# Kernel tuning notes

Measured on AMD Instinct MI355X. Metric: run time of the kernel, lower is better.

The kernel has to match this reference:

```python
import jax, jax.numpy as jnp
import numpy as np

MASK_VALUE = -1000000.0  # matches sequence_mask fill in the torch source


def setup_inputs() -> dict:
    key = jax.random.key(0)
    k1, k2, k3, k4 = jax.random.split(key, 4)
    B, Lq, Lk, D = 64, 1024, 1024, 64
    return {
        "queries": jax.random.normal(k1, (B, Lq, D), dtype=jnp.float32),
        "keys": jax.random.normal(k2, (B, Lk, D), dtype=jnp.float32),
        "values": jax.random.normal(k3, (B, Lk, D), dtype=jnp.float32),
        "valid_lens": jax.random.randint(k4, (B,), 1, Lk + 1, dtype=jnp.int64),
    }


def reference(queries, keys, values, valid_lens):
    # queries: [B, Lq, D], keys/values: [B, Lk, D], valid_lens: [B]
    d = queries.shape[-1]
    qk = jnp.einsum("bqd,bkd->bqk", queries, keys) / jnp.sqrt(jnp.asarray(d, queries.dtype))
    # sequence_mask: positions >= valid_len are set to -1e6 before softmax.
    # valid_lens is per-batch-row, broadcast over queries (repeat_interleave in torch).
    kpos = jnp.arange(keys.shape[1])  # [Lk]
    mask = kpos[None, None, :] < valid_lens[:, None, None]  # [B, 1, Lk] -> broadcast over q
    qk = jnp.where(mask, qk, jnp.asarray(MASK_VALUE, qk.dtype))
    attn = jax.nn.softmax(qk, axis=-1)
    return jnp.einsum("bqk,bkd->bqd", attn, values)
```

## Files before the change

### kernel.cpp

```cpp
#include <hip/hip_runtime.h>
#include <hip/hip_bf16.h>


#define NB    64
#define LQ    1024
#define LK    1024
#define DH    64
#define KVT   64
#define QT    128
#define NITEMS (NB * (LQ / QT))
#define NEGF  1.0e30f
#define SC2   0.18033688011112042f
#define THR   8.0f

typedef __attribute__((ext_vector_type(8))) short    bf8;
typedef __attribute__((ext_vector_type(8))) ushort   u16x8;
typedef __attribute__((ext_vector_type(4))) ushort   u16x4;
typedef __attribute__((ext_vector_type(4))) float    f4;

__device__ __forceinline__ ushort2 cvt2(float a, float b) {
    float2 f; f.x = a; f.y = b;
    __hip_bfloat162 h = __float22bfloat162_rn(f);
    union { __hip_bfloat162 h2; ushort2 u2; } u;
    u.h2 = h;
    return u.u2;
}
__device__ __forceinline__ int swz16(int row, int colbyte) {
    return row * 128 + ((((colbyte >> 4) ^ (row & 7)) << 4) | (colbyte & 15));
}
__device__ __forceinline__ int swz8(int row, int colbyte) {
    return row * 128 + ((((colbyte >> 3) ^ (row & 15)) << 3) | (colbyte & 7));
}

__global__ __launch_bounds__(512, 4)
void attn_v16(const float* __restrict__ Q, const float* __restrict__ K,
              const float* __restrict__ V, const int* __restrict__ VL,
              float* __restrict__ O) {
    __shared__ ushort KsB[2][KVT * DH];
    __shared__ ushort VtB[2][DH * KVT];
    __shared__ ushort sched[NB];

    const int tid = threadIdx.x;
    const int wid = tid >> 6, l = tid & 63, g = l >> 4, a = l & 15;

    if (tid < NB) {
        const int ntb = (VL[tid] + KVT - 1) >> 6;
        int r = 0;
        for (int j = 0; j < NB; ++j) {
            const int ntj = (VL[j] + KVT - 1) >> 6;
            r += (int)((ntj > ntb) | ((ntj == ntb) & (j < tid)));
        }
        sched[r] = (ushort)tid;
    }
    __syncthreads();
    const int xcd   = blockIdx.x & 7;
    const int slot  = blockIdx.x >> 3;
    const int qtile = slot & 7;
    const int st    = slot >> 3;
    const int rank  = xcd + ((st < 4) ? st : (11 - st)) * 8;
    const int b     = sched[rank];
    const int qbase = qtile * QT;
    const int valid = VL[b];
    const int nt = (valid + KVT - 1) >> 6;

    const float* Qr = Q + ((size_t)b * LQ + qbase + wid * 16 + a) * DH;
    bf8 qa[2];
    #pragma unroll
    for (int kblk = 0; kblk < 2; ++kblk) {
        f4 x = *(const f4*)(Qr + kblk * 32 + g * 8);
        f4 y = *(const f4*)(Qr + kblk * 32 + g * 8 + 4);
        ushort2 c0 = cvt2(x[0] * SC2, x[1] * SC2), c1 = cvt2(x[2] * SC2, x[3] * SC2);
        ushort2 c2 = cvt2(y[0] * SC2, y[1] * SC2), c3 = cvt2(y[2] * SC2, y[3] * SC2);
        qa[kblk][0] = (short)c0.x; qa[kblk][1] = (short)c0.y;
        qa[kblk][2] = (short)c1.x; qa[kblk][3] = (short)c1.y;
        qa[kblk][4] = (short)c2.x; qa[kblk][5] = (short)c2.y;
        qa[kblk][6] = (short)c3.x; qa[kblk][7] = (short)c3.y;
    }
    const bf8 ones = {0x3F80, 0x3F80, 0x3F80, 0x3F80,
                      0x3F80, 0x3F80, 0x3F80, 0x3F80};

    const int  rtid  = tid & 255;
    const bool vrole = (wid < 4);
    const int srow = rtid >> 3, sslot = rtid & 7;
    const int vkp  = rtid >> 4, vj = rtid & 15;
    const int prow = (srow & 3) | ((srow & 24) >> 1) | ((srow & 4) << 2);
    const f4* Kb4 = (const f4*)(K + (size_t)b * LK * DH);
    const f4* Vb4 = (const f4*)(V + (size_t)b * LK * DH);

    f4 r0, r1, r2, r3;
    auto load_kv = [&](int k0) {
        if (vrole) {
            r0 = Vb4[(k0 + 4 * vkp + 0) * 16 + vj];
            r1 = Vb4[(k0 + 4 * vkp + 1) * 16 + vj];
            r2 = Vb4[(k0 + 4 * vkp + 2) * 16 + vj];
            r3 = Vb4[(k0 + 4 * vkp + 3) * 16 + vj];
        } else {
            r0 = Kb4[(k0 + srow) * 16 + sslot * 2];
            r1 = Kb4[(k0 + srow) * 16 + sslot * 2 + 1];
            r2 = Kb4[(k0 + srow + 32) * 16 + sslot * 2];
            r3 = Kb4[(k0 + srow + 32) * 16 + sslot * 2 + 1];
        }
    };
    auto store_kv = [&](int bs) {
        if (vrole) {
            char* vd = (char*)&VtB[bs][0];
            #pragma unroll
            for (int c = 0; c < 4; ++c) {
                ushort2 a01 = cvt2(r0[c], r1[c]), a23 = cvt2(r2[c], r3[c]);
                u16x4 p = {a01.x, a01.y, a23.x, a23.y};
                *(u16x4*)(vd + swz8(4 * vj + c, vkp * 8)) = p;
            }
        } else {
            char* kd = (char*)&KsB[bs][0];
            {
                ushort2 c0 = cvt2(r0[0], r0[1]), c1 = cvt2(r0[2], r0[3]);
                ushort2 c2 = cvt2(r1[0], r1[1]), c3 = cvt2(r1[2], r1[3]);
                u16x8 w = {c0.x, c0.y, c1.x, c1.y, c2.x, c2.y, c3.x, c3.y};
                *(u16x8*)(kd + swz16(prow, sslot * 16)) = w;
            }
            {
                ushort2 c0 = cvt2(r2[0], r2[1]), c1 = cvt2(r2[2], r2[3]);
                ushort2 c2 = cvt2(r3[0], r3[1]), c3 = cvt2(r3[2], r3[3]);
                u16x8 w = {c0.x, c0.y, c1.x, c1.y, c2.x, c2.y, c3.x, c3.y};
                *(u16x8*)(kd + swz16(prow + 32, sslot * 16)) = w;
            }
        }
    };

    f4 oacc[4];
    #pragma unroll
    for (int n = 0; n < 4; ++n) oacc[n] = f4{0.f, 0.f, 0.f, 0.f};
    f4 lacc = f4{0.f, 0.f, 0.f, 0.f};
    float m_run = -NEGF;

    load_kv(0);
    store_kv(0);
    for (int t = 0; t < nt; ++t) {
        const int bs = t & 1;
        __syncthreads();
        if (t + 1 < nt) load_kv((t + 1) * KVT);
        __builtin_amdgcn_sched_barrier(0);

        const char* kd = (const char*)&KsB[bs][0];
        f4 sacc[4];
        #pragma unroll
        for (int n = 0; n < 4; ++n) sacc[n] = f4{0.f, 0.f, 0.f, 0.f};
        __builtin_amdgcn_s_setprio(1);
        #pragma unroll
        for (int n = 0; n < 4; ++n)
            #pragma unroll
            for (int kblk = 0; kblk < 2; ++kblk) {
                bf8 kb = *(const bf8*)(kd + swz16(n * 16 + a, kblk * 64 + g * 16));
                sacc[n] = __builtin_amdgcn_mfma_f32_16x16x32_bf16(
                    kb, qa[kblk], sacc[n], 0, 0, 0);
            }
        __builtin_amdgcn_s_setprio(0);

        float s[4][4];
        const int kmax = valid - t * KVT;
        #pragma unroll
        for (int n = 0; n < 4; ++n)
            #pragma unroll
            for (int r = 0; r < 4; ++r) s[n][r] = sacc[n][r];
        if (kmax < KVT) {
            #pragma unroll
            for (int n = 0; n < 4; ++n)
                #pragma unroll
                for (int r = 0; r < 4; ++r)
                    if (32 * (n >> 1) + 4 * (n & 1) + 8 * g + r >= kmax)
                        s[n][r] = -NEGF;
        }

        float tm = s[0][0];
        #pragma unroll
        for (int n = 0; n < 4; ++n)
            #pragma unroll
            for (int r = 0; r < 4; ++r) tm = fmaxf(tm, s[n][r]);
        tm = fmaxf(tm, __shfl_xor(tm, 16));
        tm = fmaxf(tm, __shfl_xor(tm, 32));

        float rs_ = 1.0f;
        const bool skip = __all(tm <= m_run + THR);
        if (!skip) {
            const float mnew = fmaxf(m_run, tm);
            rs_ = __builtin_exp2f(m_run - mnew);
            m_run = mnew;
        }

        float p[4][4];
        #pragma unroll
        for (int n = 0; n < 4; ++n)
            #pragma unroll
            for (int r = 0; r < 4; ++r)
                p[n][r] = __builtin_exp2f(s[n][r] - m_run);

        if (!skip) {
            float rr[4];
            #pragma unroll
            for (int r = 0; r < 4; ++r) rr[r] = __shfl(rs_, 4 * g + r);
            #pragma unroll
            for (int n = 0; n < 4; ++n)
                #pragma unroll
                for (int r = 0; r < 4; ++r) oacc[n][r] *= rr[r];
            #pragma unroll
            for (int r = 0; r < 4; ++r) lacc[r] *= rr[r];
        }

        const char* vd = (const char*)&VtB[bs][0];
        __builtin_amdgcn_s_setprio(1);
        #pragma unroll
        for (int kblk = 0; kblk < 2; ++kblk) {
            ushort2 w0 = cvt2(p[2 * kblk][0], p[2 * kblk][1]);
            ushort2 w1 = cvt2(p[2 * kblk][2], p[2 * kblk][3]);
            ushort2 w2 = cvt2(p[2 * kblk + 1][0], p[2 * kblk + 1][1]);
            ushort2 w3 = cvt2(p[2 * kblk + 1][2], p[2 * kblk + 1][3]);
            bf8 pa = {(short)w0.x, (short)w0.y, (short)w1.x, (short)w1.y,
                      (short)w2.x, (short)w2.y, (short)w3.x, (short)w3.y};
            const int cb = kblk * 64 + g * 16;
            #pragma unroll
            for (int n = 0; n < 4; ++n) {
                u16x4 lo = *(const u16x4*)(vd + swz8(n * 16 + a, cb));
                u16x4 hi = *(const u16x4*)(vd + swz8(n * 16 + a, cb + 8));
                bf8 vb_ = {(short)lo[0], (short)lo[1], (short)lo[2], (short)lo[3],
                           (short)hi[0], (short)hi[1], (short)hi[2], (short)hi[3]};
                oacc[n] = __builtin_amdgcn_mfma_f32_16x16x32_bf16(
                    pa, vb_, oacc[n], 0, 0, 0);
            }
            lacc = __builtin_amdgcn_mfma_f32_16x16x32_bf16(pa, ones, lacc, 0, 0, 0);
        }
        __builtin_amdgcn_s_setprio(0);

        if (t + 1 < nt) store_kv(bs ^ 1);
    }

    float iv[4];
    #pragma unroll
    for (int r = 0; r < 4; ++r) iv[r] = 1.0f / lacc[r];
    float* Ob = O + ((size_t)b * LQ + qbase + wid * 16) * DH;
    #pragma unroll
    for (int n = 0; n < 4; ++n)
        #pragma unroll
        for (int r = 0; r < 4; ++r)
            Ob[(size_t)(4 * g + r) * DH + 16 * n + a] = oacc[n][r] * iv[r];
}

extern "C" void kernel_launch(void* const* d_in, const int* in_sizes, int n_in,
                              void* d_out, int out_size, void* d_ws, size_t ws_size,
                              hipStream_t stream) {
    const float* Q  = (const float*)d_in[0];
    const float* K  = (const float*)d_in[1];
    const float* V  = (const float*)d_in[2];
    const int*   VL = (const int*)d_in[3];
    float* O = (float*)d_out;

    attn_v16<<<NITEMS, 512, 0, stream>>>(Q, K, V, VL, O);
}
```

Before: 33.59 us.

## Software-pipeline QK of next tile with PV of current tile

Restructures the main loop so the QK^T MFMA for tile t+1 runs right after tile t's softmax, interleaved with tile t's PV MFMA. The prologue computes the first QK, and KV loads are prefetched two tiles ahead. The aim is to let matrix work overlap the softmax exponent and reduction work. The cost is an extra barrier per iteration and more live registers. The row-max reduction is also rewritten as a balanced tree.

New measurement: 38.32 us. 1.14x slower.

```diff
diff --git a/kernel.cpp b/kernel.cpp
--- a/kernel.cpp
+++ b/kernel.cpp
@@ -33,7 +33,7 @@
 }
 
 __global__ __launch_bounds__(512, 4)
-void attn_v16(const float* __restrict__ Q, const float* __restrict__ K,
+void attn_v18(const float* __restrict__ Q, const float* __restrict__ K,
               const float* __restrict__ V, const int* __restrict__ VL,
               float* __restrict__ O) {
     __shared__ ushort KsB[2][KVT * DH];
@@ -127,25 +127,11 @@
         }
     };
 
-    f4 oacc[4];
-    #pragma unroll
-    for (int n = 0; n < 4; ++n) oacc[n] = f4{0.f, 0.f, 0.f, 0.f};
-    f4 lacc = f4{0.f, 0.f, 0.f, 0.f};
-    float m_run = -NEGF;
-
-    load_kv(0);
-    store_kv(0);
-    for (int t = 0; t < nt; ++t) {
-        const int bs = t & 1;
-        __syncthreads();
-        if (t + 1 < nt) load_kv((t + 1) * KVT);
-        __builtin_amdgcn_sched_barrier(0);
-
-        const char* kd = (const char*)&KsB[bs][0];
-        f4 sacc[4];
+    f4 sacc[4];
+    auto do_qk = [&](int bufK) {
+        const char* kd = (const char*)&KsB[bufK][0];
         #pragma unroll
         for (int n = 0; n < 4; ++n) sacc[n] = f4{0.f, 0.f, 0.f, 0.f};
-        __builtin_amdgcn_s_setprio(1);
         #pragma unroll
         for (int n = 0; n < 4; ++n)
             #pragma unroll
@@ -154,8 +140,24 @@
                 sacc[n] = __builtin_amdgcn_mfma_f32_16x16x32_bf16(
                     kb, qa[kblk], sacc[n], 0, 0, 0);
             }
-        __builtin_amdgcn_s_setprio(0);
-
+    };
+
+    f4 oacc[4];
+    #pragma unroll
+    for (int n = 0; n < 4; ++n) oacc[n] = f4{0.f, 0.f, 0.f, 0.f};
+    f4 lacc = f4{0.f, 0.f, 0.f, 0.f};
+    float m_run = -NEGF;
+
+    load_kv(0);
+    store_kv(0);
+    __syncthreads();
+    __builtin_amdgcn_s_setprio(1);
+    do_qk(0);
+    __builtin_amdgcn_s_setprio(0);
+    if (nt > 1) load_kv(KVT);
+
+    for (int t = 0; t < nt; ++t) {
+        const int bs = t & 1;
         float s[4][4];
         const int kmax = valid - t * KVT;
         #pragma unroll
@@ -171,11 +173,11 @@
                         s[n][r] = -NEGF;
         }
 
-        float tm = s[0][0];
-        #pragma unroll
-        for (int n = 0; n < 4; ++n)
-            #pragma unroll
-            for (int r = 0; r < 4; ++r) tm = fmaxf(tm, s[n][r]);
+        float m0 = fmaxf(fmaxf(s[0][0], s[0][1]), fmaxf(s[0][2], s[0][3]));
+        float m1 = fmaxf(fmaxf(s[1][0], s[1][1]), fmaxf(s[1][2], s[1][3]));
+        float m2 = fmaxf(fmaxf(s[2][0], s[2][1]), fmaxf(s[2][2], s[2][3]));
+        float m3 = fmaxf(fmaxf(s[3][0], s[3][1]), fmaxf(s[3][2], s[3][3]));
+        float tm = fmaxf(fmaxf(m0, m1), fmaxf(m2, m3));
         tm = fmaxf(tm, __shfl_xor(tm, 16));
         tm = fmaxf(tm, __shfl_xor(tm, 32));
 
@@ -206,16 +208,30 @@
             for (int r = 0; r < 4; ++r) lacc[r] *= rr[r];
         }
 
-        const char* vd = (const char*)&VtB[bs][0];
-        __builtin_amdgcn_s_setprio(1);
+        bf8 pa[2];
         #pragma unroll
         for (int kblk = 0; kblk < 2; ++kblk) {
             ushort2 w0 = cvt2(p[2 * kblk][0], p[2 * kblk][1]);
             ushort2 w1 = cvt2(p[2 * kblk][2], p[2 * kblk][3]);
             ushort2 w2 = cvt2(p[2 * kblk + 1][0], p[2 * kblk + 1][1]);
             ushort2 w3 = cvt2(p[2 * kblk + 1][2], p[2 * kblk + 1][3]);
-            bf8 pa = {(short)w0.x, (short)w0.y, (short)w1.x, (short)w1.y,
-                      (short)w2.x, (short)w2.y, (short)w3.x, (short)w3.y};
+            pa[kblk][0] = (short)w0.x; pa[kblk][1] = (short)w0.y;
+            pa[kblk][2] = (short)w1.x; pa[kblk][3] = (short)w1.y;
+            pa[kblk][4] = (short)w2.x; pa[kblk][5] = (short)w2.y;
+            pa[kblk][6] = (short)w3.x; pa[kblk][7] = (short)w3.y;
+        }
+
+        if (t + 1 < nt) store_kv(bs ^ 1);
+
+        __syncthreads();
+        if (t + 2 < nt) load_kv((t + 2) * KVT);
+        __builtin_amdgcn_sched_barrier(0);
+        __builtin_amdgcn_s_setprio(1);
+        if (t + 1 < nt) do_qk(bs ^ 1);
+
+        const char* vd = (const char*)&VtB[bs][0];
+        #pragma unroll
+        for (int kblk = 0; kblk < 2; ++kblk) {
             const int cb = kblk * 64 + g * 16;
             #pragma unroll
             for (int n = 0; n < 4; ++n) {
@@ -224,13 +240,12 @@
                 bf8 vb_ = {(short)lo[0], (short)lo[1], (short)lo[2], (short)lo[3],
                            (short)hi[0], (short)hi[1], (short)hi[2], (short)hi[3]};
                 oacc[n] = __builtin_amdgcn_mfma_f32_16x16x32_bf16(
-                    pa, vb_, oacc[n], 0, 0, 0);
-            }
-            lacc = __builtin_amdgcn_mfma_f32_16x16x32_bf16(pa, ones, lacc, 0, 0, 0);
+                    pa[kblk], vb_, oacc[n], 0, 0, 0);
+            }
+            lacc = __builtin_amdgcn_mfma_f32_16x16x32_bf16(pa[kblk], ones, lacc, 0, 0, 0);
         }
         __builtin_amdgcn_s_setprio(0);
-
-        if (t + 1 < nt) store_kv(bs ^ 1);
+        __syncthreads();
     }
 
     float iv[4];
@@ -253,5 +268,5 @@
     const int*   VL = (const int*)d_in[3];
     float* O = (float*)d_out;
 
-    attn_v16<<<NITEMS, 512, 0, stream>>>(Q, K, V, VL, O);
-}
+    attn_v18<<<NITEMS, 512, 0, stream>>>(Q, K, V, VL, O);
+}
```

## Process two 64-key KV tiles per loop iteration to halve barriers

Applied to the files above, without the earlier changes.

Each loop iteration now loads, converts and stores 128 keys/values (two 64-row halves) and computes scores and PV over both, so each barrier and online-softmax max/rescale step covers twice as much work. The exp computation is fused into the PV loop per k-block. This is meant to cut synchronisation and softmax overhead per key. In exchange it doubles LDS use (64KB per block) and register pressure, which may hurt occupancy under the 4-blocks launch bound. It also rounds the key count up to a multiple of 128, relying on masking for the extra 64-key half.

Result: slower. 38.17 us (+13.6%).

```diff
diff --git a/kernel.cpp b/kernel.cpp
--- a/kernel.cpp
+++ b/kernel.cpp
@@ -7,6 +7,7 @@
 #define LK    1024
 #define DH    64
 #define KVT   64
+#define KVP   128
 #define QT    128
 #define NITEMS (NB * (LQ / QT))
 #define NEGF  1.0e30f
@@ -33,11 +34,11 @@
 }
 
 __global__ __launch_bounds__(512, 4)
-void attn_v16(const float* __restrict__ Q, const float* __restrict__ K,
+void attn_v19(const float* __restrict__ Q, const float* __restrict__ K,
               const float* __restrict__ V, const int* __restrict__ VL,
               float* __restrict__ O) {
-    __shared__ ushort KsB[2][KVT * DH];
-    __shared__ ushort VtB[2][DH * KVT];
+    __shared__ ushort KsB[2][2][KVT * DH];
+    __shared__ ushort VtB[2][2][DH * KVT];
     __shared__ ushort sched[NB];
 
     const int tid = threadIdx.x;
@@ -62,19 +63,20 @@
     const int qbase = qtile * QT;
     const int valid = VL[b];
     const int nt = (valid + KVT - 1) >> 6;
+    const int nu = (nt + 1) >> 1;
 
     const float* Qr = Q + ((size_t)b * LQ + qbase + wid * 16 + a) * DH;
     bf8 qa[2];
     #pragma unroll
-    for (int kblk = 0; kblk < 2; ++kblk) {
-        f4 x = *(const f4*)(Qr + kblk * 32 + g * 8);
-        f4 y = *(const f4*)(Qr + kblk * 32 + g * 8 + 4);
+    for (int dk = 0; dk < 2; ++dk) {
+        f4 x = *(const f4*)(Qr + dk * 32 + g * 8);
+        f4 y = *(const f4*)(Qr + dk * 32 + g * 8 + 4);
         ushort2 c0 = cvt2(x[0] * SC2, x[1] * SC2), c1 = cvt2(x[2] * SC2, x[3] * SC2);
         ushort2 c2 = cvt2(y[0] * SC2, y[1] * SC2), c3 = cvt2(y[2] * SC2, y[3] * SC2);
-        qa[kblk][0] = (short)c0.x; qa[kblk][1] = (short)c0.y;
-        qa[kblk][2] = (short)c1.x; qa[kblk][3] = (short)c1.y;
-        qa[kblk][4] = (short)c2.x; qa[kblk][5] = (short)c2.y;
-        qa[kblk][6] = (short)c3.x; qa[kblk][7] = (short)c3.y;
+        qa[dk][0] = (short)c0.x; qa[dk][1] = (short)c0.y;
+        qa[dk][2] = (short)c1.x; qa[dk][3] = (short)c1.y;
+        qa[dk][4] = (short)c2.x; qa[dk][5] = (short)c2.y;
+        qa[dk][6] = (short)c3.x; qa[dk][7] = (short)c3.y;
     }
     const bf8 ones = {0x3F80, 0x3F80, 0x3F80, 0x3F80,
                       0x3F80, 0x3F80, 0x3F80, 0x3F80};
@@ -87,44 +89,56 @@
     const f4* Kb4 = (const f4*)(K + (size_t)b * LK * DH);
     const f4* Vb4 = (const f4*)(V + (size_t)b * LK * DH);
 
-    f4 r0, r1, r2, r3;
-    auto load_kv = [&](int k0) {
+    f4 r0, r1, r2, r3, r4, r5, r6, r7;
+    auto load_kv2 = [&](int k0) {
         if (vrole) {
             r0 = Vb4[(k0 + 4 * vkp + 0) * 16 + vj];
             r1 = Vb4[(k0 + 4 * vkp + 1) * 16 + vj];
             r2 = Vb4[(k0 + 4 * vkp + 2) * 16 + vj];
             r3 = Vb4[(k0 + 4 * vkp + 3) * 16 + vj];
+            r4 = Vb4[(k0 + 64 + 4 * vkp + 0) * 16 + vj];
+            r5 = Vb4[(k0 + 64 + 4 * vkp + 1) * 16 + vj];
+            r6 = Vb4[(k0 + 64 + 4 * vkp + 2) * 16 + vj];
+            r7 = Vb4[(k0 + 64 + 4 * vkp + 3) * 16 + vj];
         } else {
             r0 = Kb4[(k0 + srow) * 16 + sslot * 2];
             r1 = Kb4[(k0 + srow) * 16 + sslot * 2 + 1];
             r2 = Kb4[(k0 + srow + 32) * 16 + sslot * 2];
             r3 = Kb4[(k0 + srow + 32) * 16 + sslot * 2 + 1];
+            r4 = Kb4[(k0 + 64 + srow) * 16 + sslot * 2];
+            r5 = Kb4[(k0 + 64 + srow) * 16 + sslot * 2 + 1];
+            r6 = Kb4[(k0 + 64 + srow + 32) * 16 + sslot * 2];
+            r7 = Kb4[(k0 + 64 + srow + 32) * 16 + sslot * 2 + 1];
         }
     };
-    auto store_kv = [&](int bs) {
+    auto store_half = [&](int bs, int h, f4 a0, f4 a1, f4 a2, f4 a3) {
         if (vrole) {
-            char* vd = (char*)&VtB[bs][0];
+            char* vd = (char*)&VtB[bs][h][0];
             #pragma unroll
             for (int c = 0; c < 4; ++c) {
-                ushort2 a01 = cvt2(r0[c], r1[c]), a23 = cvt2(r2[c], r3[c]);
+                ushort2 a01 = cvt2(a0[c], a1[c]), a23 = cvt2(a2[c], a3[c]);
                 u16x4 p = {a01.x, a01.y, a23.x, a23.y};
                 *(u16x4*)(vd + swz8(4 * vj + c, vkp * 8)) = p;
             }
         } else {
-            char* kd = (char*)&KsB[bs][0];
+            char* kd = (char*)&KsB[bs][h][0];
             {
-                ushort2 c0 = cvt2(r0[0], r0[1]), c1 = cvt2(r0[2], r0[3]);
-                ushort2 c2 = cvt2(r1[0], r1[1]), c3 = cvt2(r1[2], r1[3]);
+                ushort2 c0 = cvt2(a0[0], a0[1]), c1 = cvt2(a0[2], a0[3]);
+                ushort2 c2 = cvt2(a1[0], a1[1]), c3 = cvt2(a1[2], a1[3]);
                 u16x8 w = {c0.x, c0.y, c1.x, c1.y, c2.x, c2.y, c3.x, c3.y};
                 *(u16x8*)(kd + swz16(prow, sslot * 16)) = w;
             }
             {
-                ushort2 c0 = cvt2(r2[0], r2[1]), c1 = cvt2(r2[2], r2[3]);
-                ushort2 c2 = cvt2(r3[0], r3[1]), c3 = cvt2(r3[2], r3[3]);
+                ushort2 c0 = cvt2(a2[0], a2[1]), c1 = cvt2(a2[2], a2[3]);
+                ushort2 c2 = cvt2(a3[0], a3[1]), c3 = cvt2(a3[2], a3[3]);
                 u16x8 w = {c0.x, c0.y, c1.x, c1.y, c2.x, c2.y, c3.x, c3.y};
                 *(u16x8*)(kd + swz16(prow + 32, sslot * 16)) = w;
             }
         }
+    };
+    auto store_kv2 = [&](int bs) {
+        store_half(bs, 0, r0, r1, r2, r3);
+        store_half(bs, 1, r4, r5, r6, r7);
     };
 
     f4 oacc[4];
@@ -133,49 +147,50 @@
     f4 lacc = f4{0.f, 0.f, 0.f, 0.f};
     float m_run = -NEGF;
 
-    load_kv(0);
-    store_kv(0);
-    for (int t = 0; t < nt; ++t) {
-        const int bs = t & 1;
+    load_kv2(0);
+    store_kv2(0);
+    for (int u = 0; u < nu; ++u) {
+        const int bs = u & 1;
         __syncthreads();
-        if (t + 1 < nt) load_kv((t + 1) * KVT);
+        if (u + 1 < nu) load_kv2((u + 1) * KVP);
         __builtin_amdgcn_sched_barrier(0);
 
-        const char* kd = (const char*)&KsB[bs][0];
-        f4 sacc[4];
-        #pragma unroll
-        for (int n = 0; n < 4; ++n) sacc[n] = f4{0.f, 0.f, 0.f, 0.f};
+        f4 sacc[8];
+        #pragma unroll
+        for (int n = 0; n < 8; ++n) sacc[n] = f4{0.f, 0.f, 0.f, 0.f};
         __builtin_amdgcn_s_setprio(1);
         #pragma unroll
-        for (int n = 0; n < 4; ++n)
-            #pragma unroll
-            for (int kblk = 0; kblk < 2; ++kblk) {
-                bf8 kb = *(const bf8*)(kd + swz16(n * 16 + a, kblk * 64 + g * 16));
+        for (int n = 0; n < 8; ++n) {
+            const char* kd = (const char*)&KsB[bs][n >> 2][0];
+            const int row = (n & 3) * 16 + a;
+            #pragma unroll
+            for (int dk = 0; dk < 2; ++dk) {
+                bf8 kb = *(const bf8*)(kd + swz16(row, dk * 64 + g * 16));
                 sacc[n] = __builtin_amdgcn_mfma_f32_16x16x32_bf16(
-                    kb, qa[kblk], sacc[n], 0, 0, 0);
-            }
+                    kb, qa[dk], sacc[n], 0, 0, 0);
+            }
+        }
         __builtin_amdgcn_s_setprio(0);
 
-        float s[4][4];
-        const int kmax = valid - t * KVT;
-        #pragma unroll
-        for (int n = 0; n < 4; ++n)
-            #pragma unroll
-            for (int r = 0; r < 4; ++r) s[n][r] = sacc[n][r];
-        if (kmax < KVT) {
-            #pragma unroll
-            for (int n = 0; n < 4; ++n)
+        const int kmax = valid - u * KVP;
+        if (kmax < KVP) {
+            #pragma unroll
+            for (int n = 0; n < 8; ++n) {
+                const int kb_ = 64 * (n >> 2) + 32 * ((n >> 1) & 1) + 4 * (n & 1);
                 #pragma unroll
                 for (int r = 0; r < 4; ++r)
-                    if (32 * (n >> 1) + 4 * (n & 1) + 8 * g + r >= kmax)
-                        s[n][r] = -NEGF;
-        }
-
-        float tm = s[0][0];
-        #pragma unroll
-        for (int n = 0; n < 4; ++n)
-            #pragma unroll
-            for (int r = 0; r < 4; ++r) tm = fmaxf(tm, s[n][r]);
+                    if (kb_ + 8 * g + r >= kmax) sacc[n][r] = -NEGF;
+            }
+        }
+
+        float mn[8];
+        #pragma unroll
+        for (int n = 0; n < 8; ++n)
+            mn[n] = fmaxf(fmaxf(sacc[n][0], sacc[n][1]),
+                          fmaxf(sacc[n][2], sacc[n][3]));
+        float t0 = fmaxf(fmaxf(mn[0], mn[1]), fmaxf(mn[2], mn[3]));
+        float t1 = fmaxf(fmaxf(mn[4], mn[5]), fmaxf(mn[6], mn[7]));
+        float tm = fmaxf(t0, t1);
         tm = fmaxf(tm, __shfl_xor(tm, 16));
         tm = fmaxf(tm, __shfl_xor(tm, 32));
 
@@ -186,14 +201,6 @@
             rs_ = __builtin_exp2f(m_run - mnew);
             m_run = mnew;
         }
-
-        float p[4][4];
-        #pragma unroll
-        for (int n = 0; n < 4; ++n)
-            #pragma unroll
-            for (int r = 0; r < 4; ++r)
-                p[n][r] = __builtin_exp2f(s[n][r] - m_run);
-
         if (!skip) {
             float rr[4];
             #pragma unroll
@@ -206,17 +213,21 @@
             for (int r = 0; r < 4; ++r) lacc[r] *= rr[r];
         }
 
-        const char* vd = (const char*)&VtB[bs][0];
         __builtin_amdgcn_s_setprio(1);
         #pragma unroll
-        for (int kblk = 0; kblk < 2; ++kblk) {
-            ushort2 w0 = cvt2(p[2 * kblk][0], p[2 * kblk][1]);
-            ushort2 w1 = cvt2(p[2 * kblk][2], p[2 * kblk][3]);
-            ushort2 w2 = cvt2(p[2 * kblk + 1][0], p[2 * kblk + 1][1]);
-            ushort2 w3 = cvt2(p[2 * kblk + 1][2], p[2 * kblk + 1][3]);
+        for (int kblk = 0; kblk < 4; ++kblk) {
+            float p0[4], p1[4];
+            #pragma unroll
+            for (int r = 0; r < 4; ++r) {
+                p0[r] = __builtin_exp2f(sacc[2 * kblk][r] - m_run);
+                p1[r] = __builtin_exp2f(sacc[2 * kblk + 1][r] - m_run);
+            }
+            ushort2 w0 = cvt2(p0[0], p0[1]), w1 = cvt2(p0[2], p0[3]);
+            ushort2 w2 = cvt2(p1[0], p1[1]), w3 = cvt2(p1[2], p1[3]);
             bf8 pa = {(short)w0.x, (short)w0.y, (short)w1.x, (short)w1.y,
                       (short)w2.x, (short)w2.y, (short)w3.x, (short)w3.y};
-            const int cb = kblk * 64 + g * 16;
+            const char* vd = (const char*)&VtB[bs][kblk >> 1][0];
+            const int cb = (kblk & 1) * 64 + g * 16;
             #pragma unroll
             for (int n = 0; n < 4; ++n) {
                 u16x4 lo = *(const u16x4*)(vd + swz8(n * 16 + a, cb));
@@ -230,7 +241,7 @@
         }
         __builtin_amdgcn_s_setprio(0);
 
-        if (t + 1 < nt) store_kv(bs ^ 1);
+        if (u + 1 < nu) store_kv2(bs ^ 1);
     }
 
     float iv[4];
@@ -253,5 +264,5 @@
     const int*   VL = (const int*)d_in[3];
     float* O = (float*)d_out;
 
-    attn_v16<<<NITEMS, 512, 0, stream>>>(Q, K, V, VL, O);
-}
+    attn_v19<<<NITEMS, 512, 0, stream>>>(Q, K, V, VL, O);
+}
```
